# Kernel tuning notes

Hardware: AMD Instinct MI355X
Metric: run time of the kernel (lower is better)

The kernel has to match this reference:

```python
import jax, jax.numpy as jnp
import numpy as np

FLOW_SCALE = 8.0  # typical pixel displacement magnitude


def setup_inputs() -> dict:
    key = jax.random.key(0)
    k1, k2, k3 = jax.random.split(key, 3)
    tenInput = jax.random.normal(k1, (4, 64, 256, 448), dtype=jnp.float32)
    tenFlow = jax.random.normal(k2, (4, 2, 256, 448), dtype=jnp.float32) * FLOW_SCALE
    tenMetric = jax.random.normal(k3, (4, 1, 256, 448), dtype=jnp.float32)
    return {"tenInput": tenInput, "tenFlow": tenFlow, "tenMetric": tenMetric}


def _softsplat_sum(vals, flow):
    # vals: [C1, H, W] augmented input, flow: [2, H, W] (x-disp, y-disp)
    C1, H, W = vals.shape
    gx = jnp.arange(W, dtype=flow.dtype)
    gy = jnp.arange(H, dtype=flow.dtype)
    fltX = gx[None, :] + flow[0]  # [H, W] target x
    fltY = gy[:, None] + flow[1]  # [H, W] target y
    x0 = jnp.floor(fltX)
    y0 = jnp.floor(fltY)
    x1 = x0 + 1.0
    y1 = y0 + 1.0
    # bilinear splat weights for the 4 neighbors
    wNW = (x1 - fltX) * (y1 - fltY)
    wNE = (fltX - x0) * (y1 - fltY)
    wSW = (x1 - fltX) * (fltY - y0)
    wSE = (fltX - x0) * (fltY - y0)
    valsf = vals.reshape(C1, H * W)
    out = jnp.zeros((C1, H * W), dtype=vals.dtype)
    for xi, yi, w in ((x0, y0, wNW), (x1, y0, wNE), (x0, y1, wSW), (x1, y1, wSE)):
        xi_i = xi.astype(jnp.int32)
        yi_i = yi.astype(jnp.int32)
        valid = (xi_i >= 0) & (xi_i < W) & (yi_i >= 0) & (yi_i < H)
        idx = jnp.where(valid, yi_i * W + xi_i, 0).reshape(-1)   # [H*W]
        wv = jnp.where(valid, w, 0.0).reshape(-1)                # [H*W]
        out = out.at[:, idx].add(valsf * wv[None, :])
    return out.reshape(C1, H, W)


def reference(tenInput, tenFlow, tenMetric):
    # strType == 'softmax': splat [input*exp(metric), exp(metric)], then normalize
    m = jnp.exp(tenMetric)                                 # [B,1,H,W]
    aug = jnp.concatenate([tenInput * m, m], axis=1)       # [B,C+1,H,W]
    out = jax.vmap(_softsplat_sum)(aug, tenFlow)           # [B,C+1,H,W]
    norm = out[:, -1:, :, :]
    norm = jnp.where(norm == 0.0, jnp.ones_like(norm), norm)
    return out[:, :-1, :, :] / norm
```

## Files before the change

kernel.cpp:

```cpp
#include <hip/hip_runtime.h>

constexpr int N = 4;
constexpr int C = 64;
constexpr int H = 256;
constexpr int W = 448;
constexpr int HW = H * W;

constexpr int TS = 16;
constexpr int TW = W / TS;
constexpr int TH = H / TS;
constexpr int TILES_PB = TW * TH;
constexpr int TILES = N * TILES_PB;


__device__ __forceinline__ int tileOf(int x, int y) {
    if ((unsigned)x >= (unsigned)W || (unsigned)y >= (unsigned)H) return -1;
    return (y >> 4) * TW + (x >> 4);
}

__device__ __forceinline__ int quadTiles(int x0, int y0, int t[4]) {
    const int x1 = x0 + 1, y1 = y0 + 1;
    const int t00 = tileOf(x0, y0), t10 = tileOf(x1, y0);
    const int t01 = tileOf(x0, y1), t11 = tileOf(x1, y1);
    int n = 0;
    if (t00 >= 0) t[n++] = t00;
    if (t10 >= 0 && t10 != t00) t[n++] = t10;
    if (t01 >= 0 && t01 != t00 && t01 != t10) t[n++] = t01;
    if (t11 >= 0 && t11 != t00 && t11 != t10 && t11 != t01) t[n++] = t11;
    return n;
}

__global__ __launch_bounds__(256) void prep_kernel(
    const float* __restrict__ input,
    const float* __restrict__ flow,
    const float* __restrict__ metric,
    float* __restrict__ aug,
    unsigned* __restrict__ counts)
{
    __shared__ float s_val[128][65];
    __shared__ float s_m[128];
    __shared__ unsigned lcnt[TILES_PB];

    const int tid = threadIdx.x;
    const int blockPix = blockIdx.x * 128;
    const int b = blockPix / HW;
    const int pb = blockPix - b * HW;

    for (int i = tid; i < TILES_PB; i += 256) lcnt[i] = 0;
    __syncthreads();

    if (tid < 128) {
        const int p = pb + tid;
        const int y = p / W;
        const int x = p - y * W;
        const float fx = (float)x + flow[(b * 2 + 0) * HW + p];
        const float fy = (float)y + flow[(b * 2 + 1) * HW + p];
        const float m = __expf(metric[b * HW + p]);
        s_m[tid] = m;

        const int x0 = (int)floorf(fx), y0 = (int)floorf(fy);
        int t[4];
        const int nt = quadTiles(x0, y0, t);
        for (int i = 0; i < nt; ++i) atomicAdd(&lcnt[t[i]], 1u);
    }

    {
        const int sp = tid & 127;
        const int sc = tid >> 7;
        const float* ib = input + (size_t)b * C * HW + pb + sp;
#pragma unroll
        for (int c = 0; c < 32; ++c) {
            const int ch = 2 * c + sc;
            s_val[sp][ch] = ib[(size_t)ch * HW];
        }
    }
    __syncthreads();

    for (int i = tid; i < TILES_PB; i += 256)
        if (lcnt[i]) atomicAdd(&counts[b * TILES_PB + i], lcnt[i]);

    const int wv = tid >> 6, ln = tid & 63;
    float* abase = aug + ((size_t)b * HW + pb) * 64;
#pragma unroll
    for (int it = 0; it < 32; ++it) {
        const int j = (wv << 5) + it;
        abase[(size_t)j * 64 + ln] = s_val[j][ln] * s_m[j];
    }
}

__global__ __launch_bounds__(256) void scan_kernel(
    const unsigned* __restrict__ counts,
    unsigned* __restrict__ segstart,
    unsigned capE)
{
    __shared__ unsigned lsum[256];
    const int tid = threadIdx.x;
    unsigned v[7];
    unsigned s = 0;
#pragma unroll
    for (int i = 0; i < 7; ++i) { v[i] = counts[tid * 7 + i]; s += v[i]; }
    lsum[tid] = s;
    __syncthreads();
    for (int off = 1; off < 256; off <<= 1) {
        const unsigned t = (tid >= off) ? lsum[tid - off] : 0u;
        __syncthreads();
        lsum[tid] += t;
        __syncthreads();
    }
    unsigned run = lsum[tid] - s;
#pragma unroll
    for (int i = 0; i < 7; ++i) {
        segstart[tid * 7 + i] = run < capE ? run : capE;
        run += v[i];
    }
    if (tid == 255) segstart[TILES] = run < capE ? run : capE;
}

__global__ __launch_bounds__(1024) void fill_kernel(
    const float* __restrict__ flow,
    const float* __restrict__ metric,
    const unsigned* __restrict__ segstart,
    unsigned* __restrict__ cursor,
    float4* __restrict__ recs,
    unsigned capE)
{
    __shared__ unsigned lcnt[TILES_PB];
    __shared__ unsigned lbase[TILES_PB];

    const int tid = threadIdx.x;
    const int idx = blockIdx.x * 1024 + tid;
    const int b = idx / HW;
    const int p = idx - b * HW;
    const int y = p / W;
    const int x = p - y * W;

    if (tid < TILES_PB) lcnt[tid] = 0;
    __syncthreads();

    const float fx = (float)x + flow[(b * 2 + 0) * HW + p];
    const float fy = (float)y + flow[(b * 2 + 1) * HW + p];
    const float m  = __expf(metric[b * HW + p]);
    const int x0 = (int)floorf(fx), y0 = (int)floorf(fy);

    int t[4];
    const int nt = quadTiles(x0, y0, t);
    unsigned lofs[4];
#pragma unroll
    for (int i = 0; i < 4; ++i)
        lofs[i] = (i < nt) ? atomicAdd(&lcnt[t[i]], 1u) : 0u;
    __syncthreads();

    const int tb = b * TILES_PB;
    if (tid < TILES_PB && lcnt[tid])
        lbase[tid] = atomicAdd(&cursor[tb + tid], lcnt[tid]);
    __syncthreads();

    const float4 rec = make_float4(fx, fy, m, __int_as_float(p));
#pragma unroll
    for (int i = 0; i < 4; ++i) {
        if (i < nt) {
            const int tt = t[i];
            const unsigned slot = segstart[tb + tt] + lbase[tt] + lofs[i];
            if (slot < capE) recs[slot] = rec;
        }
    }
}

__global__ __launch_bounds__(256) void gather2(
    const float4* __restrict__ recs,
    const float* __restrict__ aug,
    const unsigned* __restrict__ segstart,
    float* __restrict__ out)
{
    const int tid  = threadIdx.x;
    const int wq   = tid >> 6;
    const int lane = tid & 63;
    const int b  = blockIdx.x / TILES_PB;
    const int tt = blockIdx.x - b * TILES_PB;
    const int ty0 = (tt / TW) * TS;
    const int tx0 = (tt - (tt / TW) * TW) * TS;
    const int qx0 = tx0 + (wq & 1) * 8;
    const int qy0 = ty0 + (wq >> 1) * 8;

    const float fxLo = (float)qx0 - 1.0f, fxHi = (float)qx0 + 8.0f;
    const float fyLo = (float)qy0 - 1.0f, fyHi = (float)qy0 + 8.0f;
    const float X = (float)(qx0 + (lane & 7));
    const float Y = (float)(qy0 + (lane >> 3));

    float acc[64];
#pragma unroll
    for (int c = 0; c < 64; ++c) acc[c] = 0.0f;
    float nrm = 0.0f;

    const int start = (int)segstart[blockIdx.x];
    const int end   = (int)segstart[blockIdx.x + 1];
    const float* ab = aug + (size_t)b * HW * 64;

    float4 r = (start < end) ? recs[start]
                             : make_float4(-1e30f, -1e30f, 0.0f, 0.0f);
    for (int e = start; e < end; ++e) {
        float4 rn = (e + 1 < end) ? recs[e + 1]
                                  : make_float4(-1e30f, -1e30f, 0.0f, 0.0f);

        const float fx = r.x, fy = r.y, m = r.z;
        if (fx > fxLo && fx < fxHi && fy > fyLo && fy < fyHi) {
            const int p = __builtin_amdgcn_readfirstlane(__float_as_int(r.w));
            const float ax = 1.0f - fabsf(fx - X);
            const float ay = 1.0f - fabsf(fy - Y);
            const float w = fmaxf(ax, 0.0f) * fmaxf(ay, 0.0f);
            nrm = fmaf(m, w, nrm);
            const float* vp = ab + (size_t)p * 64;
#pragma unroll
            for (int c = 0; c < 64; ++c)
                acc[c] = fmaf(vp[c], w, acc[c]);
        }
        r = rn;
    }

    const float inv = (nrm == 0.0f) ? 1.0f : (1.0f / nrm);
    float* ob = out + (size_t)b * C * HW;
    const int loff = (qy0 + (lane >> 3)) * W + qx0 + (lane & 7);
#pragma unroll
    for (int c = 0; c < 64; ++c)
        ob[(size_t)c * HW + loff] = acc[c] * inv;
}

__global__ __launch_bounds__(256) void splat_nhwc(
    const float* __restrict__ input,
    const float* __restrict__ flow,
    const float* __restrict__ metric,
    float* __restrict__ scr,
    float* __restrict__ norm)
{
    __shared__ float s_val[128][65];
    __shared__ float s_fx[128], s_fy[128], s_m[128];

    const int tid = threadIdx.x;
    const int nwg = gridDim.x;
    const int bid = blockIdx.x;
    const int swz = (bid & 7) * (nwg >> 3) + (bid >> 3);

    const int blockPix = swz * 128;
    const int b = blockPix / HW;
    const int pb = blockPix - b * HW;

    if (tid < 128) {
        const int p = pb + tid;
        const int y = p / W;
        const int x = p - y * W;
        s_fx[tid] = (float)x + flow[(b * 2 + 0) * HW + p];
        s_fy[tid] = (float)y + flow[(b * 2 + 1) * HW + p];
        s_m[tid]  = __expf(metric[b * HW + p]);
    }
    {
        const int sp = tid & 127;
        const int sc = tid >> 7;
        const float* ib = input + (size_t)b * C * HW + pb + sp;
#pragma unroll
        for (int c = 0; c < 32; ++c) {
            const int ch = 2 * c + sc;
            s_val[sp][ch] = ib[(size_t)ch * HW];
        }
    }
    __syncthreads();

    const int wave = tid >> 6;
    const int lane = tid & 63;
    float* __restrict__ sb = scr + (size_t)b * HW * 64;
    float* __restrict__ nb = norm + b * HW;

    for (int k = 0; k < 32; ++k) {
        const int j = (wave << 5) | k;
        const float fx = s_fx[j], fy = s_fy[j], m = s_m[j];
        const float v = s_val[j][lane] * m;

        const float x0f = floorf(fx), y0f = floorf(fy);
        const int x0 = (int)x0f, y0 = (int)y0f;
        const int x1 = x0 + 1,   y1 = y0 + 1;
        const float wx1 = fx - x0f, wx0 = 1.0f - wx1;
        const float wy1 = fy - y0f, wy0 = 1.0f - wy1;

        const bool vx0 = (x0 >= 0) & (x0 < W);
        const bool vx1 = (x1 >= 0) & (x1 < W);
        const bool vy0 = (y0 >= 0) & (y0 < H);
        const bool vy1 = (y1 >= 0) & (y1 < H);

        if (vx0 & vy0) {
            const float w = wx0 * wy0; const int t = y0 * W + x0;
            atomicAdd(sb + (size_t)t * 64 + lane, v * w);
            if (lane == 0) atomicAdd(nb + t, m * w);
        }
        if (vx1 & vy0) {
            const float w = wx1 * wy0; const int t = y0 * W + x1;
            atomicAdd(sb + (size_t)t * 64 + lane, v * w);
            if (lane == 0) atomicAdd(nb + t, m * w);
        }
        if (vx0 & vy1) {
            const float w = wx0 * wy1; const int t = y1 * W + x0;
            atomicAdd(sb + (size_t)t * 64 + lane, v * w);
            if (lane == 0) atomicAdd(nb + t, m * w);
        }
        if (vx1 & vy1) {
            const float w = wx1 * wy1; const int t = y1 * W + x1;
            atomicAdd(sb + (size_t)t * 64 + lane, v * w);
            if (lane == 0) atomicAdd(nb + t, m * w);
        }
    }
}

__global__ __launch_bounds__(256) void untranspose_norm(
    const float* __restrict__ scr,
    const float* __restrict__ norm,
    float* __restrict__ out)
{
    __shared__ float s_t[64][65];
    __shared__ float s_inv[64];

    const int tid = threadIdx.x;
    const int strips = HW / 64;
    const int b = blockIdx.x / strips;
    const int pblk = (blockIdx.x - b * strips) * 64;

    if (tid < 64) {
        float n = norm[b * HW + pblk + tid];
        s_inv[tid] = (n == 0.0f) ? 1.0f : (1.0f / n);
    }
    const float* sb = scr + ((size_t)b * HW + pblk) * 64;
#pragma unroll
    for (int r = 0; r < 16; ++r) {
        const int pr = r * 4 + (tid >> 6);
        const int c  = tid & 63;
        s_t[pr][c] = sb[(size_t)pr * 64 + c];
    }
    __syncthreads();

    float* ob = out + (size_t)b * C * HW + pblk;
#pragma unroll
    for (int r = 0; r < 16; ++r) {
        const int c   = r * 4 + (tid >> 6);
        const int pix = tid & 63;
        ob[(size_t)c * HW + pix] = s_t[pix][c] * s_inv[pix];
    }
}

__global__ void splat_kernel(const float* __restrict__ input,
                             const float* __restrict__ flow,
                             const float* __restrict__ metric,
                             float* __restrict__ out,
                             float* __restrict__ norm)
{
    int idx = blockIdx.x * blockDim.x + threadIdx.x;
    if (idx >= N * HW) return;
    int b = idx / HW;
    int p = idx - b * HW;
    int y = p / W;
    int x = p - y * W;

    float fx = (float)x + flow[(b * 2 + 0) * HW + p];
    float fy = (float)y + flow[(b * 2 + 1) * HW + p];
    float m  = __expf(metric[b * HW + p]);

    float x0f = floorf(fx), y0f = floorf(fy);
    int x0 = (int)x0f, y0 = (int)y0f;
    int x1 = x0 + 1,   y1 = y0 + 1;
    float wx1 = fx - x0f, wx0 = 1.0f - wx1;
    float wy1 = fy - y0f, wy0 = 1.0f - wy1;

    bool vx0 = (x0 >= 0) & (x0 < W);
    bool vx1 = (x1 >= 0) & (x1 < W);
    bool vy0 = (y0 >= 0) & (y0 < H);
    bool vy1 = (y1 >= 0) & (y1 < H);

    bool vNW = vx0 & vy0, vNE = vx1 & vy0, vSW = vx0 & vy1, vSE = vx1 & vy1;
    float wNW = wx0 * wy0, wNE = wx1 * wy0, wSW = wx0 * wy1, wSE = wx1 * wy1;
    int iNW = y0 * W + x0, iNE = y0 * W + x1, iSW = y1 * W + x0, iSE = y1 * W + x1;

    {
        float* nb = norm + b * HW;
        if (vNW) atomicAdd(nb + iNW, m * wNW);
        if (vNE) atomicAdd(nb + iNE, m * wNE);
        if (vSW) atomicAdd(nb + iSW, m * wSW);
        if (vSE) atomicAdd(nb + iSE, m * wSE);
    }

    const float* ib = input + (size_t)b * C * HW + p;
    float* ob = out + (size_t)b * C * HW;
#pragma unroll 4
    for (int c = 0; c < C; ++c) {
        float v = ib[(size_t)c * HW] * m;
        float* oc = ob + (size_t)c * HW;
        if (vNW) atomicAdd(oc + iNW, v * wNW);
        if (vNE) atomicAdd(oc + iNE, v * wNE);
        if (vSW) atomicAdd(oc + iSW, v * wSW);
        if (vSE) atomicAdd(oc + iSE, v * wSE);
    }
}

__global__ void norm_kernel(float* __restrict__ out,
                            const float* __restrict__ norm)
{
    int idx = blockIdx.x * blockDim.x + threadIdx.x;
    int total = N * C * HW / 4;
    if (idx >= total) return;

    int pixq = idx % (HW / 4);
    int bc   = idx / (HW / 4);
    int b    = bc / C;

    const float4* np4 = (const float4*)(norm + (size_t)b * HW);
    float4 n = np4[pixq];
    n.x = (n.x == 0.0f) ? 1.0f : n.x;
    n.y = (n.y == 0.0f) ? 1.0f : n.y;
    n.z = (n.z == 0.0f) ? 1.0f : n.z;
    n.w = (n.w == 0.0f) ? 1.0f : n.w;

    float4* o4 = (float4*)out;
    float4 v = o4[idx];
    v.x /= n.x; v.y /= n.y; v.z /= n.z; v.w /= n.w;
    o4[idx] = v;
}

extern "C" void kernel_launch(void* const* d_in, const int* in_sizes, int n_in,
                              void* d_out, int out_size, void* d_ws, size_t ws_size,
                              hipStream_t stream)
{
    const float* input  = (const float*)d_in[0];
    const float* flow   = (const float*)d_in[1];
    const float* metric = (const float*)d_in[2];
    float* out = (float*)d_out;

    const size_t augElems  = (size_t)N * HW * 64;
    const size_t metaElems = (size_t)TILES * 2 + TILES + 1;

    const size_t capFull = (size_t)4 * N * HW;
    const size_t cap2x   = (size_t)2 * N * HW;
    const size_t cap15x  = (size_t)3 * N * HW / 2;

    auto need = [&](size_t capE) {
        return (augElems + capE * 4 + metaElems) * sizeof(float);
    };
    const size_t need_mid = (augElems + (size_t)N * HW) * sizeof(float);

    size_t capE = 0;
    if      (ws_size >= need(capFull)) capE = capFull;
    else if (ws_size >= need(cap2x))   capE = cap2x;
    else if (ws_size >= need(cap15x))  capE = cap15x;

    if (capE) {
        float*    aug      = (float*)d_ws;
        float4*   recs     = (float4*)(aug + augElems);
        unsigned* counts   = (unsigned*)(recs + capE);
        unsigned* cursor   = counts + TILES;
        unsigned* segstart = cursor + TILES;

        hipMemsetAsync(counts, 0, 2 * TILES * sizeof(unsigned), stream);
        prep_kernel<<<N * HW / 128, 256, 0, stream>>>(input, flow, metric, aug, counts);
        scan_kernel<<<1, 256, 0, stream>>>(counts, segstart, (unsigned)capE);
        fill_kernel<<<N * HW / 1024, 1024, 0, stream>>>(flow, metric, segstart, cursor,
                                                        recs, (unsigned)capE);
        gather2<<<TILES, 256, 0, stream>>>(recs, aug, segstart, out);
    } else if (ws_size >= need_mid) {
        float* scr  = (float*)d_ws;
        float* norm = scr + augElems;
        hipMemsetAsync(scr, 0, need_mid, stream);

        splat_nhwc<<<N * HW / 128, 256, 0, stream>>>(input, flow, metric, scr, norm);
        untranspose_norm<<<N * (HW / 64), 256, 0, stream>>>(scr, norm, out);
    } else {
        float* norm = (float*)d_ws;
        hipMemsetAsync(out,  0, (size_t)N * C * HW * sizeof(float), stream);
        hipMemsetAsync(norm, 0, (size_t)N * HW * sizeof(float), stream);

        splat_kernel<<<(N * HW + 255) / 256, 256, 0, stream>>>(input, flow, metric, out, norm);
        int total = N * C * HW / 4;
        norm_kernel<<<(total + 255) / 256, 256, 0, stream>>>(out, norm);
    }
}
```

Before: 434.5 us.

## Bin splats per 8x8 wavefront tile and fuse augment with record fill

Switches binning from 16x16 tiles shared by four wavefronts to 8x8 bins owned by one wavefront each. Every record in a bin now contributes, so the gather drops its per-record bounds check and no longer visits records that belong to another quadrant. A light count kernel now runs before the scan, and the augmented-value transpose is merged into the fill pass, which appends records with global atomics on per-bin cursors. The gather grid is swizzled across blocks. The trade-offs are a wider 1024-thread scan, more global atomic contention in the fill, and a flow read in two kernels.

```diff
diff --git a/kernel.cpp b/kernel.cpp
--- a/kernel.cpp
+++ b/kernel.cpp
@@ -6,48 +6,105 @@
 constexpr int W = 448;
 constexpr int HW = H * W;
 
-constexpr int TS = 16;
-constexpr int TW = W / TS;
-constexpr int TH = H / TS;
-constexpr int TILES_PB = TW * TH;
-constexpr int TILES = N * TILES_PB;
-
-
-__device__ __forceinline__ int tileOf(int x, int y) {
-    if ((unsigned)x >= (unsigned)W || (unsigned)y >= (unsigned)H) return -1;
-    return (y >> 4) * TW + (x >> 4);
-}
-
-__device__ __forceinline__ int quadTiles(int x0, int y0, int t[4]) {
+constexpr int BS = 8;
+constexpr int BW_ = W / BS;
+constexpr int BH_ = H / BS;
+constexpr int BINS_PB = BW_ * BH_;
+constexpr int BINS = N * BINS_PB;
+
+
+__device__ __forceinline__ int binsOf(int x0, int y0, int bins[4]) {
     const int x1 = x0 + 1, y1 = y0 + 1;
-    const int t00 = tileOf(x0, y0), t10 = tileOf(x1, y0);
-    const int t01 = tileOf(x0, y1), t11 = tileOf(x1, y1);
     int n = 0;
-    if (t00 >= 0) t[n++] = t00;
-    if (t10 >= 0 && t10 != t00) t[n++] = t10;
-    if (t01 >= 0 && t01 != t00 && t01 != t10) t[n++] = t01;
-    if (t11 >= 0 && t11 != t00 && t11 != t10 && t11 != t01) t[n++] = t11;
+    int bxA = -2, bxB = -2, byA = -2, byB = -2;
+    if ((unsigned)x0 < (unsigned)W) bxA = x0 >> 3;
+    if ((unsigned)x1 < (unsigned)W) { const int t = x1 >> 3; if (t != bxA) bxB = t; }
+    if ((unsigned)y0 < (unsigned)H) byA = y0 >> 3;
+    if ((unsigned)y1 < (unsigned)H) { const int t = y1 >> 3; if (t != byA) byB = t; }
+    if (byA >= 0) {
+        if (bxA >= 0) bins[n++] = byA * BW_ + bxA;
+        if (bxB >= 0) bins[n++] = byA * BW_ + bxB;
+    }
+    if (byB >= 0) {
+        if (bxA >= 0) bins[n++] = byB * BW_ + bxA;
+        if (bxB >= 0) bins[n++] = byB * BW_ + bxB;
+    }
     return n;
 }
 
-__global__ __launch_bounds__(256) void prep_kernel(
+__global__ __launch_bounds__(1024) void count_kernel(
+    const float* __restrict__ flow,
+    unsigned* __restrict__ counts)
+{
+    __shared__ unsigned lcnt[BINS_PB];
+    const int tid = threadIdx.x;
+    const int idx = blockIdx.x * 1024 + tid;
+    const int b = idx / HW;
+    const int p = idx - b * HW;
+    const int y = p / W;
+    const int x = p - y * W;
+
+    for (int i = tid; i < BINS_PB; i += 1024) lcnt[i] = 0;
+    __syncthreads();
+
+    const float fx = (float)x + flow[(b * 2 + 0) * HW + p];
+    const float fy = (float)y + flow[(b * 2 + 1) * HW + p];
+    const int x0 = (int)floorf(fx), y0 = (int)floorf(fy);
+
+    int bn[4];
+    const int nb = binsOf(x0, y0, bn);
+    for (int i = 0; i < nb; ++i) atomicAdd(&lcnt[bn[i]], 1u);
+    __syncthreads();
+
+    for (int i = tid; i < BINS_PB; i += 1024)
+        if (lcnt[i]) atomicAdd(&counts[b * BINS_PB + i], lcnt[i]);
+}
+
+__global__ __launch_bounds__(1024) void scan_kernel(
+    const unsigned* __restrict__ counts,
+    unsigned* __restrict__ segstart,
+    unsigned capE)
+{
+    __shared__ unsigned lsum[1024];
+    const int tid = threadIdx.x;
+    unsigned v[7];
+    unsigned s = 0;
+#pragma unroll
+    for (int i = 0; i < 7; ++i) { v[i] = counts[tid * 7 + i]; s += v[i]; }
+    lsum[tid] = s;
+    __syncthreads();
+    for (int off = 1; off < 1024; off <<= 1) {
+        const unsigned t = (tid >= off) ? lsum[tid - off] : 0u;
+        __syncthreads();
+        lsum[tid] += t;
+        __syncthreads();
+    }
+    unsigned run = lsum[tid] - s;
+#pragma unroll
+    for (int i = 0; i < 7; ++i) {
+        segstart[tid * 7 + i] = run < capE ? run : capE;
+        run += v[i];
+    }
+    if (tid == 1023) segstart[BINS] = run < capE ? run : capE;
+}
+
+__global__ __launch_bounds__(256) void prepfill_kernel(
     const float* __restrict__ input,
     const float* __restrict__ flow,
     const float* __restrict__ metric,
+    const unsigned* __restrict__ segstart,
+    unsigned* __restrict__ cursor,
+    float4* __restrict__ recs,
     float* __restrict__ aug,
-    unsigned* __restrict__ counts)
+    unsigned capE)
 {
     __shared__ float s_val[128][65];
     __shared__ float s_m[128];
-    __shared__ unsigned lcnt[TILES_PB];
 
     const int tid = threadIdx.x;
     const int blockPix = blockIdx.x * 128;
     const int b = blockPix / HW;
     const int pb = blockPix - b * HW;
-
-    for (int i = tid; i < TILES_PB; i += 256) lcnt[i] = 0;
-    __syncthreads();
 
     if (tid < 128) {
         const int p = pb + tid;
@@ -59,9 +116,15 @@
         s_m[tid] = m;
 
         const int x0 = (int)floorf(fx), y0 = (int)floorf(fy);
-        int t[4];
-        const int nt = quadTiles(x0, y0, t);
-        for (int i = 0; i < nt; ++i) atomicAdd(&lcnt[t[i]], 1u);
+        int bn[4];
+        const int nb = binsOf(x0, y0, bn);
+        const float4 rec = make_float4(fx, fy, m, __int_as_float(p));
+        const int tb = b * BINS_PB;
+        for (int i = 0; i < nb; ++i) {
+            const unsigned off = atomicAdd(&cursor[tb + bn[i]], 1u);
+            const unsigned slot = segstart[tb + bn[i]] + off;
+            if (slot < capE) recs[slot] = rec;
+        }
     }
 
     {
@@ -76,9 +139,6 @@
     }
     __syncthreads();
 
-    for (int i = tid; i < TILES_PB; i += 256)
-        if (lcnt[i]) atomicAdd(&counts[b * TILES_PB + i], lcnt[i]);
-
     const int wv = tid >> 6, ln = tid & 63;
     float* abase = aug + ((size_t)b * HW + pb) * 64;
 #pragma unroll
@@ -88,85 +148,7 @@
     }
 }
 
-__global__ __launch_bounds__(256) void scan_kernel(
-    const unsigned* __restrict__ counts,
-    unsigned* __restrict__ segstart,
-    unsigned capE)
-{
-    __shared__ unsigned lsum[256];
-    const int tid = threadIdx.x;
-    unsigned v[7];
-    unsigned s = 0;
-#pragma unroll
-    for (int i = 0; i < 7; ++i) { v[i] = counts[tid * 7 + i]; s += v[i]; }
-    lsum[tid] = s;
-    __syncthreads();
-    for (int off = 1; off < 256; off <<= 1) {
-        const unsigned t = (tid >= off) ? lsum[tid - off] : 0u;
-        __syncthreads();
-        lsum[tid] += t;
-        __syncthreads();
-    }
-    unsigned run = lsum[tid] - s;
-#pragma unroll
-    for (int i = 0; i < 7; ++i) {
-        segstart[tid * 7 + i] = run < capE ? run : capE;
-        run += v[i];
-    }
-    if (tid == 255) segstart[TILES] = run < capE ? run : capE;
-}
-
-__global__ __launch_bounds__(1024) void fill_kernel(
-    const float* __restrict__ flow,
-    const float* __restrict__ metric,
-    const unsigned* __restrict__ segstart,
-    unsigned* __restrict__ cursor,
-    float4* __restrict__ recs,
-    unsigned capE)
-{
-    __shared__ unsigned lcnt[TILES_PB];
-    __shared__ unsigned lbase[TILES_PB];
-
-    const int tid = threadIdx.x;
-    const int idx = blockIdx.x * 1024 + tid;
-    const int b = idx / HW;
-    const int p = idx - b * HW;
-    const int y = p / W;
-    const int x = p - y * W;
-
-    if (tid < TILES_PB) lcnt[tid] = 0;
-    __syncthreads();
-
-    const float fx = (float)x + flow[(b * 2 + 0) * HW + p];
-    const float fy = (float)y + flow[(b * 2 + 1) * HW + p];
-    const float m  = __expf(metric[b * HW + p]);
-    const int x0 = (int)floorf(fx), y0 = (int)floorf(fy);
-
-    int t[4];
-    const int nt = quadTiles(x0, y0, t);
-    unsigned lofs[4];
-#pragma unroll
-    for (int i = 0; i < 4; ++i)
-        lofs[i] = (i < nt) ? atomicAdd(&lcnt[t[i]], 1u) : 0u;
-    __syncthreads();
-
-    const int tb = b * TILES_PB;
-    if (tid < TILES_PB && lcnt[tid])
-        lbase[tid] = atomicAdd(&cursor[tb + tid], lcnt[tid]);
-    __syncthreads();
-
-    const float4 rec = make_float4(fx, fy, m, __int_as_float(p));
-#pragma unroll
-    for (int i = 0; i < 4; ++i) {
-        if (i < nt) {
-            const int tt = t[i];
-            const unsigned slot = segstart[tb + tt] + lbase[tt] + lofs[i];
-            if (slot < capE) recs[slot] = rec;
-        }
-    }
-}
-
-__global__ __launch_bounds__(256) void gather2(
+__global__ __launch_bounds__(256) void gather3(
     const float4* __restrict__ recs,
     const float* __restrict__ aug,
     const unsigned* __restrict__ segstart,
@@ -175,15 +157,19 @@
     const int tid  = threadIdx.x;
     const int wq   = tid >> 6;
     const int lane = tid & 63;
-    const int b  = blockIdx.x / TILES_PB;
-    const int tt = blockIdx.x - b * TILES_PB;
-    const int ty0 = (tt / TW) * TS;
-    const int tx0 = (tt - (tt / TW) * TW) * TS;
-    const int qx0 = tx0 + (wq & 1) * 8;
-    const int qy0 = ty0 + (wq >> 1) * 8;
-
-    const float fxLo = (float)qx0 - 1.0f, fxHi = (float)qx0 + 8.0f;
-    const float fyLo = (float)qy0 - 1.0f, fyHi = (float)qy0 + 8.0f;
+
+    const int nwg = gridDim.x;
+    const int bid = blockIdx.x;
+    const int swz = (bid & 7) * (nwg >> 3) + (bid >> 3);
+
+    const int g   = swz * 4 + wq;
+    const int b   = g / BINS_PB;
+    const int bin = g - b * BINS_PB;
+    const int by  = bin / BW_;
+    const int bx  = bin - by * BW_;
+    const int qx0 = bx * BS;
+    const int qy0 = by * BS;
+
     const float X = (float)(qx0 + (lane & 7));
     const float Y = (float)(qy0 + (lane >> 3));
 
@@ -192,28 +178,24 @@
     for (int c = 0; c < 64; ++c) acc[c] = 0.0f;
     float nrm = 0.0f;
 
-    const int start = (int)segstart[blockIdx.x];
-    const int end   = (int)segstart[blockIdx.x + 1];
+    const int start = (int)segstart[g];
+    const int end   = (int)segstart[g + 1];
     const float* ab = aug + (size_t)b * HW * 64;
 
     float4 r = (start < end) ? recs[start]
-                             : make_float4(-1e30f, -1e30f, 0.0f, 0.0f);
+                             : make_float4(0.0f, 0.0f, 0.0f, 0.0f);
     for (int e = start; e < end; ++e) {
-        float4 rn = (e + 1 < end) ? recs[e + 1]
-                                  : make_float4(-1e30f, -1e30f, 0.0f, 0.0f);
-
-        const float fx = r.x, fy = r.y, m = r.z;
-        if (fx > fxLo && fx < fxHi && fy > fyLo && fy < fyHi) {
-            const int p = __builtin_amdgcn_readfirstlane(__float_as_int(r.w));
-            const float ax = 1.0f - fabsf(fx - X);
-            const float ay = 1.0f - fabsf(fy - Y);
-            const float w = fmaxf(ax, 0.0f) * fmaxf(ay, 0.0f);
-            nrm = fmaf(m, w, nrm);
-            const float* vp = ab + (size_t)p * 64;
-#pragma unroll
-            for (int c = 0; c < 64; ++c)
-                acc[c] = fmaf(vp[c], w, acc[c]);
-        }
+        const float4 rn = (e + 1 < end) ? recs[e + 1]
+                                        : make_float4(0.0f, 0.0f, 0.0f, 0.0f);
+        const int p = __builtin_amdgcn_readfirstlane(__float_as_int(r.w));
+        const float ax = fmaxf(1.0f - fabsf(r.x - X), 0.0f);
+        const float ay = fmaxf(1.0f - fabsf(r.y - Y), 0.0f);
+        const float w = ax * ay;
+        nrm = fmaf(r.z, w, nrm);
+        const float* vp = ab + (size_t)p * 64;
+#pragma unroll
+        for (int c = 0; c < 64; ++c)
+            acc[c] = fmaf(vp[c], w, acc[c]);
         r = rn;
     }
 
@@ -429,17 +411,17 @@
     const float* metric = (const float*)d_in[2];
     float* out = (float*)d_out;
 
-    const size_t augElems  = (size_t)N * HW * 64;
-    const size_t metaElems = (size_t)TILES * 2 + TILES + 1;
+    const size_t augBytes  = (size_t)N * HW * 64 * sizeof(float);
+    const size_t metaBytes = ((size_t)BINS * 2 + BINS + 1) * sizeof(unsigned);
 
     const size_t capFull = (size_t)4 * N * HW;
     const size_t cap2x   = (size_t)2 * N * HW;
     const size_t cap15x  = (size_t)3 * N * HW / 2;
 
     auto need = [&](size_t capE) {
-        return (augElems + capE * 4 + metaElems) * sizeof(float);
+        return augBytes + capE * sizeof(float4) + metaBytes;
     };
-    const size_t need_mid = (augElems + (size_t)N * HW) * sizeof(float);
+    const size_t need_mid = augBytes + (size_t)N * HW * sizeof(float);
 
     size_t capE = 0;
     if      (ws_size >= need(capFull)) capE = capFull;
@@ -448,20 +430,21 @@
 
     if (capE) {
         float*    aug      = (float*)d_ws;
-        float4*   recs     = (float4*)(aug + augElems);
+        float4*   recs     = (float4*)((char*)d_ws + augBytes);
         unsigned* counts   = (unsigned*)(recs + capE);
-        unsigned* cursor   = counts + TILES;
-        unsigned* segstart = cursor + TILES;
-
-        hipMemsetAsync(counts, 0, 2 * TILES * sizeof(unsigned), stream);
-        prep_kernel<<<N * HW / 128, 256, 0, stream>>>(input, flow, metric, aug, counts);
-        scan_kernel<<<1, 256, 0, stream>>>(counts, segstart, (unsigned)capE);
-        fill_kernel<<<N * HW / 1024, 1024, 0, stream>>>(flow, metric, segstart, cursor,
-                                                        recs, (unsigned)capE);
-        gather2<<<TILES, 256, 0, stream>>>(recs, aug, segstart, out);
+        unsigned* cursor   = counts + BINS;
+        unsigned* segstart = cursor + BINS;
+
+        hipMemsetAsync(counts, 0, 2 * BINS * sizeof(unsigned), stream);
+        count_kernel<<<N * HW / 1024, 1024, 0, stream>>>(flow, counts);
+        scan_kernel<<<1, 1024, 0, stream>>>(counts, segstart, (unsigned)capE);
+        prepfill_kernel<<<N * HW / 128, 256, 0, stream>>>(input, flow, metric,
+                                                          segstart, cursor, recs,
+                                                          aug, (unsigned)capE);
+        gather3<<<BINS / 4, 256, 0, stream>>>(recs, aug, segstart, out);
     } else if (ws_size >= need_mid) {
         float* scr  = (float*)d_ws;
-        float* norm = scr + augElems;
+        float* norm = scr + (size_t)N * HW * 64;
         hipMemsetAsync(scr, 0, need_mid, stream);
 
         splat_nhwc<<<N * HW / 128, 256, 0, stream>>>(input, flow, metric, scr, norm);
```

New measurement: 719.6 us. 65.6% more time.
